# Kernel optimization log

Measured on AMD Instinct MI355X. Metric: run time of the kernel, lower is better.

## Reference

```python
import jax, jax.numpy as jnp
import numpy as np

SUBDIVISIONS = 3  # init_kwargs
EPS = 1e-6


def setup_inputs() -> dict:
    key = jax.random.key(0)
    k1, k2, k3 = jax.random.split(key, 3)
    V, K, F = 100000, 32, 64
    features = jax.random.normal(k1, (V, F), dtype=jnp.float32)
    distsq = jax.random.uniform(k2, (V, K), dtype=jnp.float32)
    neighbour_indices = jax.random.randint(k3, (V, K), 0, V, dtype=jnp.int32)
    length_scale = jnp.float32(1.0)  # non-trainable Variable, init 1.0
    return {"features": features, "distsq": distsq,
            "neighbour_indices": neighbour_indices, "length_scale": length_scale}


def reference(features, distsq, neighbour_indices, length_scale):
    # Inference path: no length-scale EMA update (training=None -> in_train_phase takes the
    # unchanged value), distsq is stop-gradient.
    distsq = jax.lax.stop_gradient(distsq)
    scaler = 10.0 * length_scale * float(SUBDIVISIONS)
    d = jnp.sqrt(distsq + EPS)                      # (V, K) neighbor distances
    nfeat = features[neighbour_indices]             # (V, K, F) gathered neighbor features
    outs = []
    for i in range(SUBDIVISIONS):
        offset = float(i) / length_scale            # radius-bin center
        w = jnp.exp(-scaler * (d - offset) ** 2)    # (V, K) Gaussian radius-bin weights
        num = jnp.einsum('vk,vkf->vf', w, nfeat)    # weighted sum over neighbors
        den = jnp.sum(w, axis=1, keepdims=True) + EPS
        outs.append(num / den)                      # soft-pixel weighted mean
    return jnp.concatenate(outs, axis=1)            # (V, SUBDIVISIONS * F)
```

## Files before the change

### kernel.cpp

```cpp
#include <hip/hip_runtime.h>

#define SP_EPS 1e-6f
typedef __fp16 h2 __attribute__((ext_vector_type(2)));

__global__ __launch_bounds__(256) void f32_to_f16_kernel(
    const float* __restrict__ in, unsigned* __restrict__ outh, int n4)
{
    int i = blockIdx.x * 256 + threadIdx.x;
    if (i >= n4) return;
    const float4 v = ((const float4*)in)[i];
    h2 p0 = __builtin_amdgcn_cvt_pkrtz(v.x, v.y);
    h2 p1 = __builtin_amdgcn_cvt_pkrtz(v.z, v.w);
    uint2 o;
    o.x = *(unsigned*)&p0;
    o.y = *(unsigned*)&p1;
    ((uint2*)outh)[i] = o;
}

__global__ __launch_bounds__(256) void softpixel_mix_kernel(
    const unsigned short* __restrict__ fb,
    const float* __restrict__ distsq,
    const int*   __restrict__ nidx,
    const float* __restrict__ ls_ptr,
    float*       __restrict__ out,
    int V)
{
    __shared__ float4 qbuf[4][32];
    const int lane = threadIdx.x & 63;
    const int wv   = threadIdx.x >> 6;
    const int v    = blockIdx.x * 4 + wv;
    const int h    = lane >> 5;
    const int j    = lane & 31;
    const int vc   = v < V ? v : V - 1;

    const float ls     = ls_ptr[0];
    const float scaler = 30.0f * ls;
    const float inv_ls = 1.0f / ls;

    const unsigned dvoff = (unsigned)vc * 32u + (unsigned)j;
    const float dsq = distsq[dvoff];
    const int   nb  = nidx[dvoff];
    const float d   = sqrtf(dsq + SP_EPS);
    const float t1  = d - inv_ls;
    const float t2  = d - 2.0f * inv_ls;
    const float w0  = __expf(-scaler * d  * d);
    const float w1  = __expf(-scaler * t1 * t1);
    const float w2  = __expf(-scaler * t2 * t2);
    if (h == 0)
        qbuf[wv][j] = make_float4(__int_as_float(nb), w0, w1, w2);
    __syncthreads();

    float a0l = 0.f, a0h = 0.f, a1l = 0.f, a1h = 0.f, a2l = 0.f, a2h = 0.f;
    const unsigned j4 = (unsigned)(j << 2);

    #pragma unroll
    for (int kk = 0; kk < 16; ++kk) {
        const float4 q = qbuf[wv][2 * kk + h];
        const int    ik = __float_as_int(q.x);
        const unsigned boff = ((unsigned)ik << 7) + j4;
        const unsigned fp = *(const unsigned*)((const char*)fb + boff);
        asm("v_fma_mix_f32 %0, %1, %2, %0 op_sel:[0,0,0] op_sel_hi:[0,1,0]"
            : "+v"(a0l) : "v"(q.y), "v"(fp));
        asm("v_fma_mix_f32 %0, %1, %2, %0 op_sel:[0,1,0] op_sel_hi:[0,1,0]"
            : "+v"(a0h) : "v"(q.y), "v"(fp));
        asm("v_fma_mix_f32 %0, %1, %2, %0 op_sel:[0,0,0] op_sel_hi:[0,1,0]"
            : "+v"(a1l) : "v"(q.z), "v"(fp));
        asm("v_fma_mix_f32 %0, %1, %2, %0 op_sel:[0,1,0] op_sel_hi:[0,1,0]"
            : "+v"(a1h) : "v"(q.z), "v"(fp));
        asm("v_fma_mix_f32 %0, %1, %2, %0 op_sel:[0,0,0] op_sel_hi:[0,1,0]"
            : "+v"(a2l) : "v"(q.w), "v"(fp));
        asm("v_fma_mix_f32 %0, %1, %2, %0 op_sel:[0,1,0] op_sel_hi:[0,1,0]"
            : "+v"(a2h) : "v"(q.w), "v"(fp));
    }

    float s0 = w0, s1 = w1, s2 = w2;
    #pragma unroll
    for (int st = 1; st < 32; st <<= 1) {
        s0 += __shfl_xor(s0, st, 64);
        s1 += __shfl_xor(s1, st, 64);
        s2 += __shfl_xor(s2, st, 64);
    }
    const float r0 = __builtin_amdgcn_rcpf(s0 + SP_EPS);
    const float r1 = __builtin_amdgcn_rcpf(s1 + SP_EPS);
    const float r2 = __builtin_amdgcn_rcpf(s2 + SP_EPS);

    asm("v_permlane32_swap_b32 %0, %1" : "+v"(a0l), "+v"(a0h));
    asm("v_permlane32_swap_b32 %0, %1" : "+v"(a1l), "+v"(a1h));
    asm("v_permlane32_swap_b32 %0, %1" : "+v"(a2l), "+v"(a2h));
    const float c0 = a0l + a0h;
    const float c1 = a1l + a1h;
    const float c2 = a2l + a2h;

    if (v < V) {
        float* o = out + (unsigned)v * 192u + (unsigned)((j << 1) + h);
        o[0]   = c0 * r0;
        o[64]  = c1 * r1;
        o[128] = c2 * r2;
    }
}

__global__ __launch_bounds__(256) void softpixel_f32_kernel(
    const float* __restrict__ feat,
    const float* __restrict__ distsq,
    const int*   __restrict__ nidx,
    const float* __restrict__ ls_ptr,
    float*       __restrict__ out,
    int V)
{
    const int lane = threadIdx.x & 63;
    const int wv   = threadIdx.x >> 6;
    const int v    = blockIdx.x * 4 + wv;
    if (v >= V) return;

    const float ls     = ls_ptr[0];
    const float scaler = 30.0f * ls;
    const float inv_ls = 1.0f / ls;

    float w0 = 0.f, w1 = 0.f, w2 = 0.f;
    int nb = 0;
    if (lane < 32) {
        const float dsq = distsq[v * 32 + lane];
        nb = nidx[v * 32 + lane];
        const float d  = sqrtf(dsq + SP_EPS);
        const float t1 = d - inv_ls;
        const float t2 = d - 2.0f * inv_ls;
        w0 = __expf(-scaler * d  * d);
        w1 = __expf(-scaler * t1 * t1);
        w2 = __expf(-scaler * t2 * t2);
    }

    float a0 = 0.f, a1 = 0.f, a2 = 0.f;
    float s0 = SP_EPS, s1 = SP_EPS, s2 = SP_EPS;
    #pragma unroll
    for (int k = 0; k < 32; ++k) {
        const int   ik = __shfl(nb, k, 64);
        const float u0 = __shfl(w0, k, 64);
        const float u1 = __shfl(w1, k, 64);
        const float u2 = __shfl(w2, k, 64);
        const float f  = feat[(size_t)ik * 64 + lane];
        a0 = fmaf(u0, f, a0);
        a1 = fmaf(u1, f, a1);
        a2 = fmaf(u2, f, a2);
        s0 += u0; s1 += u1; s2 += u2;
    }
    float* o = out + (size_t)v * 192 + lane;
    o[0]   = a0 / s0;
    o[64]  = a1 / s1;
    o[128] = a2 / s2;
}

extern "C" void kernel_launch(void* const* d_in, const int* in_sizes, int n_in,
                              void* d_out, int out_size, void* d_ws, size_t ws_size,
                              hipStream_t stream) {
    const float* feat   = (const float*)d_in[0];
    const float* distsq = (const float*)d_in[1];
    const int*   nidx   = (const int*)d_in[2];
    const float* ls     = (const float*)d_in[3];

    const int V = in_sizes[1] / 32;
    const int F = in_sizes[0] / V;
    float* out = (float*)d_out;

    const size_t need = (size_t)V * F * sizeof(unsigned short);
    const int grid = (V + 3) / 4;

    if ((size_t)ws_size >= need && F == 64) {
        unsigned* fh = (unsigned*)d_ws;
        const int n4 = V * F / 4;
        f32_to_f16_kernel<<<(n4 + 255) / 256, 256, 0, stream>>>(feat, fh, n4);
        softpixel_mix_kernel<<<grid, 256, 0, stream>>>(
            (const unsigned short*)fh, distsq, nidx, ls, out, V);
    } else {
        softpixel_f32_kernel<<<grid, 256, 0, stream>>>(feat, distsq, nidx, ls, out, V);
    }
}
```

Measured before the change: 73.05 us.

## Split each wave into four neighbour groups with 8-byte gathers and packed FMAs

The main kernel now gives each group of 16 lanes every fourth neighbour, and each lane loads 8 bytes (4 half features) per neighbour instead of 4 bytes. The inner loop drops from 16 to 8 iterations and replaces the v_fma_mix instructions with packed v_pk_fma_f32 on fp16 values converted to fp32. Partial sums are reduced across the quarter-waves with xor shuffles, and three of the four groups each write one weight bin as a float4 store. This halves the number of gather instructions and makes the output stores wider, at the cost of explicit fp16-to-fp32 conversions and more reduction shuffles.

After: 74.58 us. 2.1% more time.

```diff
diff --git a/kernel.cpp b/kernel.cpp
--- a/kernel.cpp
+++ b/kernel.cpp
@@ -2,6 +2,16 @@
 
 #define SP_EPS 1e-6f
 typedef __fp16 h2 __attribute__((ext_vector_type(2)));
+typedef float f32x2 __attribute__((ext_vector_type(2)));
+
+struct __align__(16) QEntry { f32x2 a;  f32x2 b; };
+
+__device__ __forceinline__ f32x2 shflx2(f32x2 x, int m) {
+    f32x2 r;
+    r.x = __shfl_xor(x.x, m, 64);
+    r.y = __shfl_xor(x.y, m, 64);
+    return r;
+}
 
 __global__ __launch_bounds__(256) void f32_to_f16_kernel(
     const float* __restrict__ in, unsigned* __restrict__ outh, int n4)
@@ -17,7 +27,7 @@
     ((uint2*)outh)[i] = o;
 }
 
-__global__ __launch_bounds__(256) void softpixel_mix_kernel(
+__global__ __launch_bounds__(256) void softpixel_qw_kernel(
     const unsigned short* __restrict__ fb,
     const float* __restrict__ distsq,
     const int*   __restrict__ nidx,
@@ -25,19 +35,20 @@
     float*       __restrict__ out,
     int V)
 {
-    __shared__ float4 qbuf[4][32];
+    __shared__ QEntry qbuf[4][32];
     const int lane = threadIdx.x & 63;
     const int wv   = threadIdx.x >> 6;
     const int v    = blockIdx.x * 4 + wv;
-    const int h    = lane >> 5;
-    const int j    = lane & 31;
+    const int q    = lane >> 4;
+    const int j    = lane & 15;
+    const int j32  = lane & 31;
     const int vc   = v < V ? v : V - 1;
 
     const float ls     = ls_ptr[0];
     const float scaler = 30.0f * ls;
     const float inv_ls = 1.0f / ls;
 
-    const unsigned dvoff = (unsigned)vc * 32u + (unsigned)j;
+    const unsigned dvoff = (unsigned)vc * 32u + (unsigned)j32;
     const float dsq = distsq[dvoff];
     const int   nb  = nidx[dvoff];
     const float d   = sqrtf(dsq + SP_EPS);
@@ -46,31 +57,42 @@
     const float w0  = __expf(-scaler * d  * d);
     const float w1  = __expf(-scaler * t1 * t1);
     const float w2  = __expf(-scaler * t2 * t2);
-    if (h == 0)
-        qbuf[wv][j] = make_float4(__int_as_float(nb), w0, w1, w2);
+    if (lane < 32) {
+        QEntry e;
+        e.a = (f32x2){w0, __int_as_float(nb)};
+        e.b = (f32x2){w1, w2};
+        qbuf[wv][j32] = e;
+    }
     __syncthreads();
 
-    float a0l = 0.f, a0h = 0.f, a1l = 0.f, a1h = 0.f, a2l = 0.f, a2h = 0.f;
-    const unsigned j4 = (unsigned)(j << 2);
+    f32x2 a01_0 = {0.f, 0.f}, a23_0 = {0.f, 0.f};
+    f32x2 a01_1 = {0.f, 0.f}, a23_1 = {0.f, 0.f};
+    f32x2 a01_2 = {0.f, 0.f}, a23_2 = {0.f, 0.f};
+    const unsigned j8 = (unsigned)(j << 3);
 
     #pragma unroll
-    for (int kk = 0; kk < 16; ++kk) {
-        const float4 q = qbuf[wv][2 * kk + h];
-        const int    ik = __float_as_int(q.x);
-        const unsigned boff = ((unsigned)ik << 7) + j4;
-        const unsigned fp = *(const unsigned*)((const char*)fb + boff);
-        asm("v_fma_mix_f32 %0, %1, %2, %0 op_sel:[0,0,0] op_sel_hi:[0,1,0]"
-            : "+v"(a0l) : "v"(q.y), "v"(fp));
-        asm("v_fma_mix_f32 %0, %1, %2, %0 op_sel:[0,1,0] op_sel_hi:[0,1,0]"
-            : "+v"(a0h) : "v"(q.y), "v"(fp));
-        asm("v_fma_mix_f32 %0, %1, %2, %0 op_sel:[0,0,0] op_sel_hi:[0,1,0]"
-            : "+v"(a1l) : "v"(q.z), "v"(fp));
-        asm("v_fma_mix_f32 %0, %1, %2, %0 op_sel:[0,1,0] op_sel_hi:[0,1,0]"
-            : "+v"(a1h) : "v"(q.z), "v"(fp));
-        asm("v_fma_mix_f32 %0, %1, %2, %0 op_sel:[0,0,0] op_sel_hi:[0,1,0]"
-            : "+v"(a2l) : "v"(q.w), "v"(fp));
-        asm("v_fma_mix_f32 %0, %1, %2, %0 op_sel:[0,1,0] op_sel_hi:[0,1,0]"
-            : "+v"(a2h) : "v"(q.w), "v"(fp));
+    for (int kk = 0; kk < 8; ++kk) {
+        const QEntry e = qbuf[wv][4 * kk + q];
+        const int ik = __float_as_int(e.a.y);
+        const unsigned boff = ((unsigned)ik << 7) + j8;
+        const uint2 fp = *(const uint2*)((const char*)fb + boff);
+        h2 pa, pb;
+        *(unsigned*)&pa = fp.x;
+        *(unsigned*)&pb = fp.y;
+        f32x2 f01; f01.x = (float)pa[0]; f01.y = (float)pa[1];
+        f32x2 f23; f23.x = (float)pb[0]; f23.y = (float)pb[1];
+        asm("v_pk_fma_f32 %0, %1, %2, %0 op_sel:[0,0,0] op_sel_hi:[0,1,1]"
+            : "+v"(a01_0) : "v"(e.a), "v"(f01));
+        asm("v_pk_fma_f32 %0, %1, %2, %0 op_sel:[0,0,0] op_sel_hi:[0,1,1]"
+            : "+v"(a23_0) : "v"(e.a), "v"(f23));
+        asm("v_pk_fma_f32 %0, %1, %2, %0 op_sel:[0,0,0] op_sel_hi:[0,1,1]"
+            : "+v"(a01_1) : "v"(e.b), "v"(f01));
+        asm("v_pk_fma_f32 %0, %1, %2, %0 op_sel:[0,0,0] op_sel_hi:[0,1,1]"
+            : "+v"(a23_1) : "v"(e.b), "v"(f23));
+        asm("v_pk_fma_f32 %0, %1, %2, %0 op_sel:[1,0,0] op_sel_hi:[1,1,1]"
+            : "+v"(a01_2) : "v"(e.b), "v"(f01));
+        asm("v_pk_fma_f32 %0, %1, %2, %0 op_sel:[1,0,0] op_sel_hi:[1,1,1]"
+            : "+v"(a23_2) : "v"(e.b), "v"(f23));
     }
 
     float s0 = w0, s1 = w1, s2 = w2;
@@ -84,18 +106,21 @@
     const float r1 = __builtin_amdgcn_rcpf(s1 + SP_EPS);
     const float r2 = __builtin_amdgcn_rcpf(s2 + SP_EPS);
 
-    asm("v_permlane32_swap_b32 %0, %1" : "+v"(a0l), "+v"(a0h));
-    asm("v_permlane32_swap_b32 %0, %1" : "+v"(a1l), "+v"(a1h));
-    asm("v_permlane32_swap_b32 %0, %1" : "+v"(a2l), "+v"(a2h));
-    const float c0 = a0l + a0h;
-    const float c1 = a1l + a1h;
-    const float c2 = a2l + a2h;
-
-    if (v < V) {
-        float* o = out + (unsigned)v * 192u + (unsigned)((j << 1) + h);
-        o[0]   = c0 * r0;
-        o[64]  = c1 * r1;
-        o[128] = c2 * r2;
+    a01_0 += shflx2(a01_0, 16);  a01_0 += shflx2(a01_0, 32);
+    a23_0 += shflx2(a23_0, 16);  a23_0 += shflx2(a23_0, 32);
+    a01_1 += shflx2(a01_1, 16);  a01_1 += shflx2(a01_1, 32);
+    a23_1 += shflx2(a23_1, 16);  a23_1 += shflx2(a23_1, 32);
+    a01_2 += shflx2(a01_2, 16);  a01_2 += shflx2(a01_2, 32);
+    a23_2 += shflx2(a23_2, 16);  a23_2 += shflx2(a23_2, 32);
+
+    if (v < V && q < 3) {
+        f32x2 o01, o23;
+        float r;
+        if (q == 0)      { o01 = a01_0; o23 = a23_0; r = r0; }
+        else if (q == 1) { o01 = a01_1; o23 = a23_1; r = r1; }
+        else             { o01 = a01_2; o23 = a23_2; r = r2; }
+        float4 ov = make_float4(o01.x * r, o01.y * r, o23.x * r, o23.y * r);
+        *(float4*)(out + (unsigned)v * 192u + (unsigned)(q << 6) + (unsigned)(j << 2)) = ov;
     }
 }
 
@@ -168,7 +193,7 @@
         unsigned* fh = (unsigned*)d_ws;
         const int n4 = V * F / 4;
         f32_to_f16_kernel<<<(n4 + 255) / 256, 256, 0, stream>>>(feat, fh, n4);
-        softpixel_mix_kernel<<<grid, 256, 0, stream>>>(
+        softpixel_qw_kernel<<<grid, 256, 0, stream>>>(
             (const unsigned short*)fh, distsq, nidx, ls, out, V);
     } else {
         softpixel_f32_kernel<<<grid, 256, 0, stream>>>(feat, distsq, nidx, ls, out, V);
```
